# Kernel optimization log

Hardware: AMD Instinct MI355X
Metric: run time of the kernel (lower is better)

The kernel has to match this reference:

```python
import jax, jax.numpy as jnp
import numpy as np

T, B = 128, 512
OBS_DIM = 512
HIDDEN = 512
ACTION_DIM = 18
LN_EPS = 1e-6  # flax LayerNorm default


def _layer_norm(x, scale, bias):
    m = jnp.mean(x, axis=-1, keepdims=True)
    v = jnp.var(x, axis=-1, keepdims=True)
    return (x - m) * jax.lax.rsqrt(v + LN_EPS) * scale + bias


def setup_inputs() -> dict:
    key = jax.random.key(0)
    ks = jax.random.split(key, 16)
    sc = lambda k, sh: jax.random.normal(k, sh, jnp.float32) * (1.0 / np.sqrt(sh[0]))
    d = {}
    d['hidden'] = jax.random.normal(ks[0], (B, HIDDEN), jnp.float32)
    d['obs'] = jax.random.normal(ks[1], (T, B, OBS_DIM), jnp.float32)
    d['dones'] = jax.random.randint(ks[2], (T, B), 0, 2).astype(bool)
    d['last_acts'] = jax.random.randint(ks[3], (T, B), 0, ACTION_DIM, dtype=jnp.int32)
    in0 = OBS_DIM + ACTION_DIM
    d['w0'] = sc(ks[4], (in0, HIDDEN)); d['b0'] = jnp.zeros((HIDDEN,), jnp.float32)
    d['ln0_s'] = jnp.ones((HIDDEN,), jnp.float32); d['ln0_b'] = jnp.zeros((HIDDEN,), jnp.float32)
    d['w1'] = sc(ks[5], (HIDDEN, HIDDEN)); d['b1'] = jnp.zeros((HIDDEN,), jnp.float32)
    d['ln1_s'] = jnp.ones((HIDDEN,), jnp.float32); d['ln1_b'] = jnp.zeros((HIDDEN,), jnp.float32)
    d['w_ir'] = sc(ks[6], (HIDDEN, HIDDEN)); d['b_ir'] = jnp.zeros((HIDDEN,), jnp.float32)
    d['w_iz'] = sc(ks[7], (HIDDEN, HIDDEN)); d['b_iz'] = jnp.zeros((HIDDEN,), jnp.float32)
    d['w_in'] = sc(ks[8], (HIDDEN, HIDDEN)); d['b_in'] = jnp.zeros((HIDDEN,), jnp.float32)
    d['w_hr'] = sc(ks[9], (HIDDEN, HIDDEN))
    d['w_hz'] = sc(ks[10], (HIDDEN, HIDDEN))
    d['w_hn'] = sc(ks[11], (HIDDEN, HIDDEN)); d['b_hn'] = jnp.zeros((HIDDEN,), jnp.float32)
    d['w_out'] = sc(ks[12], (HIDDEN, ACTION_DIM)); d['b_out'] = jnp.zeros((ACTION_DIM,), jnp.float32)
    return d


def reference(hidden, obs, dones, last_acts,
              w0, b0, ln0_s, ln0_b, w1, b1, ln1_s, ln1_b,
              w_ir, b_ir, w_iz, b_iz, w_in, b_in,
              w_hr, w_hz, w_hn, b_hn, w_out, b_out):
    # embed last actions and concat with obs: [T, B, obs_dim + action_dim]
    one_hot = jax.nn.one_hot(last_acts, ACTION_DIM, dtype=obs.dtype)
    x = jnp.concatenate([obs, one_hot], axis=-1)
    # MLP encoder: Dense -> LayerNorm -> relu, applied over all (T, B) at once
    x = jax.nn.relu(_layer_norm(x @ w0 + b0, ln0_s, ln0_b))
    x = jax.nn.relu(_layer_norm(x @ w1 + b1, ln1_s, ln1_b))

    # ScannedRNN: GRUCell with reset-to-zero carry on done, scanned over time
    def step(h, xs):
        xt, dt = xs  # xt: [B, H], dt: [B] bool
        h = jnp.where(dt[:, None], jnp.zeros_like(h), h)
        r = jax.nn.sigmoid(xt @ w_ir + b_ir + h @ w_hr)
        z = jax.nn.sigmoid(xt @ w_iz + b_iz + h @ w_hz)
        n = jnp.tanh(xt @ w_in + b_in + r * (h @ w_hn + b_hn))
        h_new = (1.0 - z) * n + z * h
        return h_new, h_new

    new_hidden, y = jax.lax.scan(step, hidden, (x, dones))
    q_vals = y @ w_out + b_out  # [T, B, action_dim]
    return new_hidden, q_vals
```

## Files before the change

kernel.cpp:

```cpp
#include <hip/hip_runtime.h>
#include <cstdint>
#include <cstddef>


#define TT 128
#define BBATCH 512
#define HH 512
#define MM 65536
#define AD 18
#define GSTEPS 8
#define FSTRIDE 32
#define READY_U32 1064960

typedef __attribute__((ext_vector_type(8))) short short8;
typedef __attribute__((ext_vector_type(4))) float float4v;
typedef __attribute__((ext_vector_type(4))) unsigned int uint4v;

__device__ __forceinline__ unsigned short f2bf(float f) {
  union { float f; unsigned int u; } v; v.f = f;
  unsigned int r = v.u + 0x7fffu + ((v.u >> 16) & 1u);
  return (unsigned short)(r >> 16);
}
__device__ __forceinline__ float bf2f(unsigned short h) {
  union { unsigned int u; float f; } v; v.u = ((unsigned int)h) << 16;
  return v.f;
}

__device__ __forceinline__ unsigned int load_u32_coh(const unsigned int* p) {
  unsigned int v;
  asm volatile("global_load_dword %0, %1, off sc0 sc1\n\ts_waitcnt vmcnt(0)"
               : "=v"(v) : "v"(p) : "memory");
  return v;
}
__device__ __forceinline__ void store_u32_coh(unsigned int* p, unsigned int v) {
  asm volatile("global_store_dword %0, %1, off sc0 sc1"
               :: "v"(p), "v"(v) : "memory");
}
__device__ __forceinline__ void store_u64_coh(void* p, unsigned long long v) {
  asm volatile("global_store_dwordx2 %0, %1, off sc0 sc1"
               :: "v"(p), "v"(v) : "memory");
}

typedef __attribute__((address_space(3))) unsigned int* lds_u32p;
typedef const __attribute__((address_space(1))) unsigned int* glb_u32p;
__device__ __forceinline__ void async16(void* lds, const void* g) {
  __builtin_amdgcn_global_load_lds(
      (glb_u32p)(unsigned long long)g,
      (lds_u32p)(unsigned int)(unsigned long long)lds, 16, 0, 0);
}


__global__ __launch_bounds__(256) void k_conv_obs(
    const float* __restrict__ src, unsigned short* __restrict__ dst,
    unsigned int* __restrict__ flag) {
  if (blockIdx.x == 0 && threadIdx.x == 0) *flag = 0u;
  int i = blockIdx.x * 256 + threadIdx.x;
  float4v v = ((const float4v*)src)[i];
  unsigned long long pk = (unsigned long long)f2bf(v[0])
      | ((unsigned long long)f2bf(v[1]) << 16)
      | ((unsigned long long)f2bf(v[2]) << 32)
      | ((unsigned long long)f2bf(v[3]) << 48);
  ((unsigned long long*)dst)[i] = pk;
}

__global__ __launch_bounds__(256) void k_prep_t(
    const float* __restrict__ w0, const float* __restrict__ w1,
    const float* __restrict__ wir, const float* __restrict__ wiz,
    const float* __restrict__ win,
    unsigned short* __restrict__ W0at, unsigned short* __restrict__ W1t,
    unsigned short* __restrict__ Wit) {
  int o = blockIdx.x * 256 + threadIdx.x;
  int n = o >> 9, k = o & 511;
  int z = blockIdx.y;
  const float* s = (z == 0) ? w0 : (z == 1) ? w1 : (z == 2) ? wir
                 : (z == 3) ? wiz : win;
  unsigned short b = f2bf(s[k * 512 + n]);
  if (z == 0) W0at[o] = b;
  else if (z == 1) W1t[o] = b;
  else Wit[(size_t)(z - 2) * 262144 + o] = b;
}

__global__ __launch_bounds__(256) void k_prep_whf(
    const float* __restrict__ whr, const float* __restrict__ whz,
    const float* __restrict__ whn, unsigned short* __restrict__ Whf) {
  int i = blockIdx.x * 256 + threadIdx.x;
  int k = i / 1536, n = i - k * 1536;
  const float* s = (n < 512) ? whr : (n < 1024) ? whz : whn;
  float v = s[k * 512 + (n & 511)];
  Whf[((size_t)(k >> 3) * 1536 + n) * 8 + (k & 7)] = f2bf(v);
}

__global__ __launch_bounds__(256) void k_prep_misc(
    const float* __restrict__ w0, const float* __restrict__ bir,
    const float* __restrict__ biz, const float* __restrict__ bin,
    const float* __restrict__ wout, const float* __restrict__ hidden,
    const int* __restrict__ dI,
    unsigned short* __restrict__ w0act, float* __restrict__ gib,
    unsigned short* __restrict__ WoutT, unsigned short* __restrict__ hbuf,
    unsigned int* __restrict__ flag) {
  int i = blockIdx.x * 256 + threadIdx.x;
  if (i < 9216) {
    int a = i >> 9, n = i & 511;
    w0act[i] = f2bf(w0[(512 + a) * 512 + n]);
  }
  if (i < 1536)
    gib[i] = (i < 512) ? bir[i] : (i < 1024) ? biz[i - 512] : bin[i - 1024];
  if (i < 32768) {
    int n = i >> 9, k = i & 511;
    WoutT[i] = f2bf(n < AD ? wout[k * AD + n] : 0.f);
  }
  if (i < 262144) hbuf[i] = f2bf(hidden[i]);
  if (i < 16384) { if (dI[i] & 0xFFFFFFFE) atomicOr(flag, 1u); }
}

__global__ __launch_bounds__(256) void k_zero(unsigned int* __restrict__ p) {
  int i = (blockIdx.x * 256 + threadIdx.x) * 4;
  if (i < READY_U32) *(uint4v*)(p + i) = (uint4v){0u, 0u, 0u, 0u};
}


template <int MODE>
__global__ __launch_bounds__(256) void k_gemm_bt(
    const unsigned short* __restrict__ Ab,
    const unsigned short* __restrict__ Btb,
    unsigned short* __restrict__ Cb,
    int Ndim, const float* __restrict__ bias,
    const unsigned short* __restrict__ gW,
    const int* __restrict__ acts) {
  __shared__ unsigned short As[8192];
  __shared__ unsigned short Bs[8192];
  const int tid = threadIdx.x, wave = tid >> 6, lane = tid & 63;
  const int quad = lane >> 4, l15 = lane & 15;
  const int m0 = blockIdx.x * 128, n0 = blockIdx.y * 128;
  const int mblk = (wave & 1) * 64, nblk = (wave >> 1) * 64;

  float4v acc[4][4];
#pragma unroll
  for (int a = 0; a < 4; ++a)
#pragma unroll
    for (int b = 0; b < 4; ++b) acc[a][b] = (float4v){0.f, 0.f, 0.f, 0.f};

  for (int k0 = 0; k0 < 512; k0 += 64) {
#pragma unroll
    for (int r = 0; r < 4; ++r) {
      int u = r * 256 + wave * 64 + lane;
      int ch = u >> 7, mm = u & 127;
      async16(&As[(size_t)(r * 256 + wave * 64) * 8],
              Ab + (size_t)(m0 + mm) * 512 + k0 + ch * 8);
      async16(&Bs[(size_t)(r * 256 + wave * 64) * 8],
              Btb + (size_t)(n0 + mm) * 512 + k0 + ch * 8);
    }
    __syncthreads();
#pragma unroll
    for (int kk = 0; kk < 2; ++kk) {
      short8 afr[4], bfr[4];
#pragma unroll
      for (int mi = 0; mi < 4; ++mi)
        afr[mi] = *(const short8*)
            &As[((kk * 4 + quad) * 128 + mblk + mi * 16 + l15) * 8];
#pragma unroll
      for (int ni = 0; ni < 4; ++ni)
        bfr[ni] = *(const short8*)
            &Bs[((kk * 4 + quad) * 128 + nblk + ni * 16 + l15) * 8];
#pragma unroll
      for (int mi = 0; mi < 4; ++mi)
#pragma unroll
        for (int ni = 0; ni < 4; ++ni)
          acc[mi][ni] = __builtin_amdgcn_mfma_f32_16x16x32_bf16(
              afr[mi], bfr[ni], acc[mi][ni], 0, 0, 0);
    }
    __syncthreads();
  }

#pragma unroll
  for (int mi = 0; mi < 4; ++mi) {
#pragma unroll
    for (int i = 0; i < 4; ++i) {
      int row = m0 + mblk + mi * 16 + quad * 4 + i;
      int arow = (MODE == 1) ? acts[row] : 0;
#pragma unroll
      for (int ni = 0; ni < 4; ++ni) {
        int col = n0 + nblk + ni * 16 + l15;
        float v = acc[mi][ni][i] + bias[col];
        if (MODE == 1) v += bf2f(gW[arow * 512 + col]);
        if (MODE == 2) {
          int t = row >> 9, b = row & 511;
          int c = col & 511;
          size_t dst = ((size_t)((b >> 6) * 32 + (c >> 4)) * 128 + t) * 3072
                     + (size_t)(col >> 9) * 1024 + (b & 63) * 16 + (c & 15);
          Cb[dst] = f2bf(v);
        } else {
          Cb[(size_t)row * Ndim + col] = f2bf(v);
        }
      }
    }
  }
}


__global__ __launch_bounds__(256) void k_ln_relu(
    const unsigned short* __restrict__ X, unsigned short* __restrict__ Y,
    const float* __restrict__ sc, const float* __restrict__ bi) {
  int row = blockIdx.x * 4 + (threadIdx.x >> 6);
  int lane = threadIdx.x & 63;
  uint4v u = *(const uint4v*)(X + (size_t)row * 512 + lane * 8);
  float v[8];
#pragma unroll
  for (int j = 0; j < 4; ++j) {
    v[2 * j] = bf2f((unsigned short)(u[j] & 0xffffu));
    v[2 * j + 1] = bf2f((unsigned short)(u[j] >> 16));
  }
  float s = 0.f, q = 0.f;
#pragma unroll
  for (int j = 0; j < 8; ++j) { s += v[j]; q += v[j] * v[j]; }
#pragma unroll
  for (int d = 1; d < 64; d <<= 1) {
    s += __shfl_xor(s, d, 64);
    q += __shfl_xor(q, d, 64);
  }
  float mean = s * (1.f / 512.f);
  float var = fmaxf(q * (1.f / 512.f) - mean * mean, 0.f);
  float rstd = rsqrtf(var + 1e-6f);
  float4v s0 = *(const float4v*)(sc + lane * 8);
  float4v s1 = *(const float4v*)(sc + lane * 8 + 4);
  float4v c0 = *(const float4v*)(bi + lane * 8);
  float4v c1 = *(const float4v*)(bi + lane * 8 + 4);
  uint4v w;
#pragma unroll
  for (int j = 0; j < 4; ++j) {
    float a0 = fmaxf((v[2 * j] - mean) * rstd * (j < 2 ? s0[2 * j] : s1[2 * j - 4])
                         + (j < 2 ? c0[2 * j] : c1[2 * j - 4]), 0.f);
    float a1 = fmaxf((v[2 * j + 1] - mean) * rstd
                         * (j < 2 ? s0[2 * j + 1] : s1[2 * j - 3])
                         + (j < 2 ? c0[2 * j + 1] : c1[2 * j - 3]), 0.f);
    w[j] = (unsigned int)f2bf(a0) | ((unsigned int)f2bf(a1) << 16);
  }
  *(uint4v*)(Y + (size_t)row * 512 + lane * 8) = w;
}


__global__ __launch_bounds__(256, 1) void k_gru(
    const unsigned short* __restrict__ Whf, const unsigned short* __restrict__ gin,
    const float* __restrict__ bhn, const int* __restrict__ dI,
    const unsigned char* __restrict__ dB, const unsigned int* __restrict__ flag,
    const unsigned short* __restrict__ hbuf, unsigned short* __restrict__ ybuf,
    float* __restrict__ outh, unsigned int* __restrict__ ready) {
  __shared__ __align__(16) unsigned short gin_lds[2][GSTEPS * 3 * 64 * 16];
  __shared__ unsigned char d_lds[TT * 64];

  const int tid = threadIdx.x, wave = tid >> 6, lane = tid & 63;
  const int quad = lane >> 4, l15 = lane & 15;
  const int rt = blockIdx.x & 7;
  const int cc = blockIdx.x >> 3;
  const int r0b = rt * 64;
  const int rowb = wave * 16 + l15;
  const int row = r0b + rowb;
  const int c0 = cc * 16 + quad * 4;
  const int bytemode = (int)(*flag);
  const float4v bhn4 = *(const float4v*)(bhn + c0);

  const unsigned short* gsrc = gin + (size_t)(rt * 32 + cc) * 128 * 3072;

  auto stage_gin = [&](int buf, int t0) {
    const unsigned short* src = gsrc + (size_t)t0 * 3072;
#pragma unroll
    for (int r = 0; r < 12; ++r) {
      async16(&gin_lds[buf][(size_t)(r * 256 + wave * 64) * 8],
              src + (size_t)(r * 256 + tid) * 8);
    }
  };

  stage_gin(0, 0);
#pragma unroll
  for (int r = 0; r < 32; ++r) {
    int idx = r * 256 + tid;
    int t = idx >> 6, rr = idx & 63;
    int gidx = t * 512 + r0b + rr;
    d_lds[idx] = bytemode ? dB[gidx] : (unsigned char)(dI[gidx] != 0);
  }

  short8 bw[3][16];
#pragma unroll
  for (int kc = 0; kc < 16; ++kc)
#pragma unroll
    for (int g = 0; g < 3; ++g) {
      size_t u = (size_t)(kc * 4 + quad) * 1536 + (g * 512 + cc * 16 + l15);
      bw[g][kc] = *(const short8*)(Whf + u * 8);
    }

  float hprev[4];
  {
    unsigned long long w = *(const unsigned long long*)(hbuf + (size_t)row * 512 + c0);
#pragma unroll
    for (int i = 0; i < 4; ++i) hprev[i] = bf2f((unsigned short)(w >> (16 * i)));
  }

  __syncthreads();

  for (int t = 0; t < TT; ++t) {
    if (t > 0) {
      if (wave == 0) {
        const unsigned int* fp =
            ready + (((size_t)rt * 130 + t) * 32 + (lane & 31)) * FSTRIDE;
        unsigned int v;
        int guard = 0;
        do {
          v = load_u32_coh(fp);
        } while (__ballot(v == 0u) != 0ull && ++guard < (1 << 22));
      }
      __syncthreads();
      asm volatile("" ::: "memory");
    }

    const unsigned short* hsrc =
        (t == 0) ? hbuf : ybuf + (size_t)(t - 1) * 262144;
    const unsigned short* ap = hsrc + (size_t)row * 512 + quad * 8;
    short8 af[16];
#pragma unroll
    for (int kc = 0; kc < 16; ++kc) af[kc] = *(const short8*)(ap + kc * 32);

    const int dd = (int)d_lds[(t << 6) + rowb];
    if (dd) {
      const short8 z8 = {0, 0, 0, 0, 0, 0, 0, 0};
#pragma unroll
      for (int kc = 0; kc < 16; ++kc) af[kc] = z8;
    }

    if ((t & (GSTEPS - 1)) == 0 && t + GSTEPS < TT)
      stage_gin(((t >> 3) + 1) & 1, t + GSTEPS);

    const int sl = t & (GSTEPS - 1), bufc = (t >> 3) & 1;
    float gr[4], gz[4], gn[4];
    {
      const unsigned short* gl =
          &gin_lds[bufc][((size_t)(sl * 3) * 64 + rowb) * 16 + quad * 4];
      unsigned long long w0 = *(const unsigned long long*)(gl);
      unsigned long long w1 = *(const unsigned long long*)(gl + 1024);
      unsigned long long w2 = *(const unsigned long long*)(gl + 2048);
#pragma unroll
      for (int i = 0; i < 4; ++i) {
        gr[i] = bf2f((unsigned short)(w0 >> (16 * i)));
        gz[i] = bf2f((unsigned short)(w1 >> (16 * i)));
        gn[i] = bf2f((unsigned short)(w2 >> (16 * i)));
      }
    }

    float4v a0 = {0.f, 0.f, 0.f, 0.f}, a1 = a0, a2 = a0;
#pragma unroll
    for (int kc = 0; kc < 16; ++kc) {
      a0 = __builtin_amdgcn_mfma_f32_16x16x32_bf16(bw[0][kc], af[kc], a0, 0, 0, 0);
      a1 = __builtin_amdgcn_mfma_f32_16x16x32_bf16(bw[1][kc], af[kc], a1, 0, 0, 0);
      a2 = __builtin_amdgcn_mfma_f32_16x16x32_bf16(bw[2][kc], af[kc], a2, 0, 0, 0);
    }

    unsigned short* ydst = ybuf + (size_t)t * 262144;
    float hv[4];
#pragma unroll
    for (int i = 0; i < 4; ++i) {
      float hold = dd ? 0.f : hprev[i];
      float r = 1.f / (1.f + __expf(-(a0[i] + gr[i])));
      float z = 1.f / (1.f + __expf(-(a1[i] + gz[i])));
      float npre = gn[i] + r * (a2[i] + bhn4[i]);
      float n = 1.f - 2.f / (1.f + __expf(2.f * npre));
      hv[i] = (1.f - z) * n + z * hold;
      hprev[i] = hv[i];
    }
    {
      unsigned long long pk = (unsigned long long)f2bf(hv[0])
          | ((unsigned long long)f2bf(hv[1]) << 16)
          | ((unsigned long long)f2bf(hv[2]) << 32)
          | ((unsigned long long)f2bf(hv[3]) << 48);
      store_u64_coh(ydst + (size_t)row * 512 + c0, pk);
    }
    if (t == TT - 1) {
      float4v o = {hv[0], hv[1], hv[2], hv[3]};
      *(float4v*)(outh + (size_t)row * 512 + c0) = o;
    }

    __syncthreads();
    if (tid == 0)
      store_u32_coh(&ready[(((size_t)rt * 130 + t + 1) * 32 + cc) * FSTRIDE], 1u);
  }
}


__global__ __launch_bounds__(256) void k_qout(
    const unsigned short* __restrict__ Yb, const unsigned short* __restrict__ Wt,
    const float* __restrict__ bout, float* __restrict__ Q) {
  __shared__ unsigned short As[8192];
  __shared__ unsigned short Bs[4096];
  const int tid = threadIdx.x, wave = tid >> 6, lane = tid & 63;
  const int quad = lane >> 4, l15 = lane & 15;
  const int m0 = blockIdx.x * 128;

  float4v acc[2][4];
#pragma unroll
  for (int a = 0; a < 2; ++a)
#pragma unroll
    for (int b = 0; b < 4; ++b) acc[a][b] = (float4v){0.f, 0.f, 0.f, 0.f};

  for (int k0 = 0; k0 < 512; k0 += 64) {
#pragma unroll
    for (int r = 0; r < 4; ++r) {
      int u = r * 256 + wave * 64 + lane;
      int ch = u >> 7, mm = u & 127;
      async16(&As[(size_t)(r * 256 + wave * 64) * 8],
              Yb + (size_t)(m0 + mm) * 512 + k0 + ch * 8);
    }
#pragma unroll
    for (int r = 0; r < 2; ++r) {
      int u = r * 256 + wave * 64 + lane;
      int ch = u >> 6, nn = u & 63;
      async16(&Bs[(size_t)(r * 256 + wave * 64) * 8],
              Wt + (size_t)nn * 512 + k0 + ch * 8);
    }
    __syncthreads();
#pragma unroll
    for (int kk = 0; kk < 2; ++kk) {
      short8 afr[2], bfr[4];
#pragma unroll
      for (int mi = 0; mi < 2; ++mi)
        afr[mi] = *(const short8*)
            &As[((kk * 4 + quad) * 128 + wave * 32 + mi * 16 + l15) * 8];
#pragma unroll
      for (int ni = 0; ni < 4; ++ni)
        bfr[ni] = *(const short8*)
            &Bs[((kk * 4 + quad) * 64 + ni * 16 + l15) * 8];
#pragma unroll
      for (int mi = 0; mi < 2; ++mi)
#pragma unroll
        for (int ni = 0; ni < 4; ++ni)
          acc[mi][ni] = __builtin_amdgcn_mfma_f32_16x16x32_bf16(
              afr[mi], bfr[ni], acc[mi][ni], 0, 0, 0);
    }
    __syncthreads();
  }
#pragma unroll
  for (int mi = 0; mi < 2; ++mi)
#pragma unroll
    for (int ni = 0; ni < 4; ++ni)
#pragma unroll
      for (int i = 0; i < 4; ++i) {
        int row = m0 + wave * 32 + mi * 16 + quad * 4 + i;
        int colq = ni * 16 + l15;
        if (colq < AD) Q[(size_t)row * AD + colq] = acc[mi][ni][i] + bout[colq];
      }
}


extern "C" void kernel_launch(void* const* d_in, const int* in_sizes, int n_in,
                              void* d_out, int out_size, void* d_ws,
                              size_t ws_size, hipStream_t stream) {
  const float* hidden = (const float*)d_in[0];
  const float* obs = (const float*)d_in[1];
  const void* dones = d_in[2];
  const int* acts = (const int*)d_in[3];
  const float* w0 = (const float*)d_in[4];
  const float* b0 = (const float*)d_in[5];
  const float* ln0s = (const float*)d_in[6];
  const float* ln0b = (const float*)d_in[7];
  const float* w1 = (const float*)d_in[8];
  const float* b1 = (const float*)d_in[9];
  const float* ln1s = (const float*)d_in[10];
  const float* ln1b = (const float*)d_in[11];
  const float* wir = (const float*)d_in[12];
  const float* bir = (const float*)d_in[13];
  const float* wiz = (const float*)d_in[14];
  const float* biz = (const float*)d_in[15];
  const float* win = (const float*)d_in[16];
  const float* bin = (const float*)d_in[17];
  const float* whr = (const float*)d_in[18];
  const float* whz = (const float*)d_in[19];
  const float* whn = (const float*)d_in[20];
  const float* bhn = (const float*)d_in[21];
  const float* wout = (const float*)d_in[22];
  const float* bout = (const float*)d_in[23];

  char* ws = (char*)d_ws;
  unsigned short* bufA = (unsigned short*)(ws);
  unsigned short* bufB = (unsigned short*)(ws + 67108864ULL);
  unsigned short* gin = (unsigned short*)(ws + 134217728ULL);
  char* D = ws + 134217728ULL + 201326592ULL;
  unsigned short* W0at = (unsigned short*)(D);
  unsigned short* W1t = (unsigned short*)(D + 524288);
  unsigned short* Wit = (unsigned short*)(D + 1048576);
  unsigned short* Whf = (unsigned short*)(D + 2621440);
  unsigned short* WoutT = (unsigned short*)(D + 4194304);
  unsigned short* w0act = (unsigned short*)(D + 4259840);
  float* gib = (float*)(D + 4292608);
  unsigned short* hbuf = (unsigned short*)(D + 4300800);
  unsigned int* flag = (unsigned int*)(D + 4825088);
  unsigned int* ready = (unsigned int*)ws;

  (void)in_sizes; (void)n_in; (void)out_size; (void)ws_size;

  k_conv_obs<<<32768, 256, 0, stream>>>(obs, bufA, flag);
  k_prep_t<<<dim3(1024, 5), 256, 0, stream>>>(w0, w1, wir, wiz, win, W0at, W1t, Wit);
  k_prep_whf<<<3072, 256, 0, stream>>>(whr, whz, whn, Whf);
  k_prep_misc<<<1024, 256, 0, stream>>>(w0, bir, biz, bin, wout, hidden,
                                        (const int*)dones, w0act, gib, WoutT,
                                        hbuf, flag);
  k_gemm_bt<1><<<dim3(512, 4), 256, 0, stream>>>(bufA, W0at, bufB, 512, b0, w0act, acts);
  k_ln_relu<<<16384, 256, 0, stream>>>(bufB, bufA, ln0s, ln0b);
  k_gemm_bt<0><<<dim3(512, 4), 256, 0, stream>>>(bufA, W1t, bufB, 512, b1, nullptr, nullptr);
  k_ln_relu<<<16384, 256, 0, stream>>>(bufB, bufA, ln1s, ln1b);
  k_gemm_bt<2><<<dim3(512, 12), 256, 0, stream>>>(bufA, Wit, gin, 1536, gib, nullptr, nullptr);
  k_zero<<<1041, 256, 0, stream>>>(ready);
  k_gru<<<256, 256, 0, stream>>>(Whf, gin, bhn, (const int*)dones,
                                 (const unsigned char*)dones, flag, hbuf, bufB,
                                 (float*)d_out, ready);
  k_qout<<<512, 256, 0, stream>>>(bufB, WoutT, bout, (float*)d_out + 262144);
}
```

Measured before the change: 1.255 ms.

## Fuse LayerNorm+ReLU into encoder GEMMs with full-row 128x512 tiles

Replaces the 128x128-tile GEMM plus separate LayerNorm kernels with a 512-thread kernel where each block computes a full 128x512 output row-tile. This lets the LayerNorm statistics be reduced in-block through shared memory and the ReLU applied before writing, so the bf16 intermediate no longer makes an extra round trip through global memory and two launches disappear. The trade-off is a larger B tile in LDS (about 64KB plus 16KB for A), more accumulator registers per thread, one block per CU and fewer blocks in flight.

```diff
diff --git a/kernel.cpp b/kernel.cpp
--- a/kernel.cpp
+++ b/kernel.cpp
@@ -120,122 +120,156 @@
 
 
 template <int MODE>
-__global__ __launch_bounds__(256) void k_gemm_bt(
+__global__ __launch_bounds__(512, 1) void k_enc(
     const unsigned short* __restrict__ Ab,
     const unsigned short* __restrict__ Btb,
     unsigned short* __restrict__ Cb,
-    int Ndim, const float* __restrict__ bias,
+    const float* __restrict__ bias,
+    const float* __restrict__ lnS, const float* __restrict__ lnB,
     const unsigned short* __restrict__ gW,
     const int* __restrict__ acts) {
   __shared__ unsigned short As[8192];
-  __shared__ unsigned short Bs[8192];
+  __shared__ unsigned short Bs[32768];
+  __shared__ float part[128][4][2];
+  __shared__ float stats[128][2];
+
   const int tid = threadIdx.x, wave = tid >> 6, lane = tid & 63;
   const int quad = lane >> 4, l15 = lane & 15;
-  const int m0 = blockIdx.x * 128, n0 = blockIdx.y * 128;
-  const int mblk = (wave & 1) * 64, nblk = (wave >> 1) * 64;
-
-  float4v acc[4][4];
+  const int wm = wave >> 2, wn = wave & 3;
+  const int m0 = blockIdx.x * 128;
+  const int g = (MODE == 2) ? blockIdx.y : 0;
+  const unsigned short* Bt = Btb + (size_t)g * 262144;
+  const float* bi = bias + g * 512;
+
+  float4v acc[4][8];
 #pragma unroll
   for (int a = 0; a < 4; ++a)
 #pragma unroll
-    for (int b = 0; b < 4; ++b) acc[a][b] = (float4v){0.f, 0.f, 0.f, 0.f};
+    for (int b = 0; b < 8; ++b) acc[a][b] = (float4v){0.f, 0.f, 0.f, 0.f};
 
   for (int k0 = 0; k0 < 512; k0 += 64) {
 #pragma unroll
-    for (int r = 0; r < 4; ++r) {
-      int u = r * 256 + wave * 64 + lane;
+    for (int r = 0; r < 2; ++r) {
+      int u = r * 512 + tid;
       int ch = u >> 7, mm = u & 127;
-      async16(&As[(size_t)(r * 256 + wave * 64) * 8],
+      async16(&As[(size_t)(r * 512 + wave * 64) * 8],
               Ab + (size_t)(m0 + mm) * 512 + k0 + ch * 8);
-      async16(&Bs[(size_t)(r * 256 + wave * 64) * 8],
-              Btb + (size_t)(n0 + mm) * 512 + k0 + ch * 8);
+    }
+#pragma unroll
+    for (int r = 0; r < 8; ++r) {
+      int u = r * 512 + tid;
+      int ch = u >> 9, nn = u & 511;
+      async16(&Bs[(size_t)(r * 512 + wave * 64) * 8],
+              Bt + (size_t)nn * 512 + k0 + ch * 8);
     }
     __syncthreads();
 #pragma unroll
     for (int kk = 0; kk < 2; ++kk) {
-      short8 afr[4], bfr[4];
+      short8 afr[4], bfr[8];
 #pragma unroll
       for (int mi = 0; mi < 4; ++mi)
         afr[mi] = *(const short8*)
-            &As[((kk * 4 + quad) * 128 + mblk + mi * 16 + l15) * 8];
-#pragma unroll
-      for (int ni = 0; ni < 4; ++ni)
+            &As[((kk * 4 + quad) * 128 + wm * 64 + mi * 16 + l15) * 8];
+#pragma unroll
+      for (int ni = 0; ni < 8; ++ni)
         bfr[ni] = *(const short8*)
-            &Bs[((kk * 4 + quad) * 128 + nblk + ni * 16 + l15) * 8];
+            &Bs[((kk * 4 + quad) * 512 + wn * 128 + ni * 16 + l15) * 8];
 #pragma unroll
       for (int mi = 0; mi < 4; ++mi)
 #pragma unroll
-        for (int ni = 0; ni < 4; ++ni)
+        for (int ni = 0; ni < 8; ++ni)
           acc[mi][ni] = __builtin_amdgcn_mfma_f32_16x16x32_bf16(
               afr[mi], bfr[ni], acc[mi][ni], 0, 0, 0);
     }
     __syncthreads();
   }
 
-#pragma unroll
-  for (int mi = 0; mi < 4; ++mi) {
+  float bcol[8];
+#pragma unroll
+  for (int ni = 0; ni < 8; ++ni) bcol[ni] = bi[wn * 128 + ni * 16 + l15];
+#pragma unroll
+  for (int mi = 0; mi < 4; ++mi)
 #pragma unroll
     for (int i = 0; i < 4; ++i) {
-      int row = m0 + mblk + mi * 16 + quad * 4 + i;
-      int arow = (MODE == 1) ? acts[row] : 0;
-#pragma unroll
-      for (int ni = 0; ni < 4; ++ni) {
-        int col = n0 + nblk + ni * 16 + l15;
-        float v = acc[mi][ni][i] + bias[col];
-        if (MODE == 1) v += bf2f(gW[arow * 512 + col]);
-        if (MODE == 2) {
-          int t = row >> 9, b = row & 511;
-          int c = col & 511;
+      int row = m0 + wm * 64 + mi * 16 + quad * 4 + i;
+      int arow = (MODE == 0) ? acts[row] : 0;
+#pragma unroll
+      for (int ni = 0; ni < 8; ++ni) {
+        float v = acc[mi][ni][i] + bcol[ni];
+        if (MODE == 0) v += bf2f(gW[arow * 512 + wn * 128 + ni * 16 + l15]);
+        acc[mi][ni][i] = v;
+      }
+    }
+
+  if (MODE <= 1) {
+#pragma unroll
+    for (int mi = 0; mi < 4; ++mi)
+#pragma unroll
+      for (int i = 0; i < 4; ++i) {
+        float s = 0.f, q = 0.f;
+#pragma unroll
+        for (int ni = 0; ni < 8; ++ni) {
+          float v = acc[mi][ni][i];
+          s += v; q += v * v;
+        }
+#pragma unroll
+        for (int d = 1; d < 16; d <<= 1) {
+          s += __shfl_xor(s, d, 64);
+          q += __shfl_xor(q, d, 64);
+        }
+        if (l15 == 0) {
+          int rowl = wm * 64 + mi * 16 + quad * 4 + i;
+          part[rowl][wn][0] = s;
+          part[rowl][wn][1] = q;
+        }
+      }
+    __syncthreads();
+    if (tid < 128) {
+      float s = part[tid][0][0] + part[tid][1][0] + part[tid][2][0] + part[tid][3][0];
+      float q = part[tid][0][1] + part[tid][1][1] + part[tid][2][1] + part[tid][3][1];
+      float mean = s * (1.f / 512.f);
+      float var = fmaxf(q * (1.f / 512.f) - mean * mean, 0.f);
+      stats[tid][0] = mean;
+      stats[tid][1] = rsqrtf(var + 1e-6f);
+    }
+    __syncthreads();
+    float sc8[8], cb8[8];
+#pragma unroll
+    for (int ni = 0; ni < 8; ++ni) {
+      int col = wn * 128 + ni * 16 + l15;
+      sc8[ni] = lnS[col];
+      cb8[ni] = lnB[col];
+    }
+#pragma unroll
+    for (int mi = 0; mi < 4; ++mi)
+#pragma unroll
+      for (int i = 0; i < 4; ++i) {
+        int rowl = wm * 64 + mi * 16 + quad * 4 + i;
+        float mean = stats[rowl][0], rstd = stats[rowl][1];
+        int row = m0 + rowl;
+#pragma unroll
+        for (int ni = 0; ni < 8; ++ni) {
+          int col = wn * 128 + ni * 16 + l15;
+          float v = fmaxf((acc[mi][ni][i] - mean) * rstd * sc8[ni] + cb8[ni], 0.f);
+          Cb[(size_t)row * 512 + col] = f2bf(v);
+        }
+      }
+  } else {
+#pragma unroll
+    for (int mi = 0; mi < 4; ++mi)
+#pragma unroll
+      for (int i = 0; i < 4; ++i) {
+        int row = m0 + wm * 64 + mi * 16 + quad * 4 + i;
+        int t = row >> 9, b = row & 511;
+#pragma unroll
+        for (int ni = 0; ni < 8; ++ni) {
+          int c = wn * 128 + ni * 16 + l15;
           size_t dst = ((size_t)((b >> 6) * 32 + (c >> 4)) * 128 + t) * 3072
-                     + (size_t)(col >> 9) * 1024 + (b & 63) * 16 + (c & 15);
-          Cb[dst] = f2bf(v);
-        } else {
-          Cb[(size_t)row * Ndim + col] = f2bf(v);
+                     + (size_t)g * 1024 + (b & 63) * 16 + (c & 15);
+          Cb[dst] = f2bf(acc[mi][ni][i]);
         }
       }
-    }
-  }
-}
-
-
-__global__ __launch_bounds__(256) void k_ln_relu(
-    const unsigned short* __restrict__ X, unsigned short* __restrict__ Y,
-    const float* __restrict__ sc, const float* __restrict__ bi) {
-  int row = blockIdx.x * 4 + (threadIdx.x >> 6);
-  int lane = threadIdx.x & 63;
-  uint4v u = *(const uint4v*)(X + (size_t)row * 512 + lane * 8);
-  float v[8];
-#pragma unroll
-  for (int j = 0; j < 4; ++j) {
-    v[2 * j] = bf2f((unsigned short)(u[j] & 0xffffu));
-    v[2 * j + 1] = bf2f((unsigned short)(u[j] >> 16));
-  }
-  float s = 0.f, q = 0.f;
-#pragma unroll
-  for (int j = 0; j < 8; ++j) { s += v[j]; q += v[j] * v[j]; }
-#pragma unroll
-  for (int d = 1; d < 64; d <<= 1) {
-    s += __shfl_xor(s, d, 64);
-    q += __shfl_xor(q, d, 64);
-  }
-  float mean = s * (1.f / 512.f);
-  float var = fmaxf(q * (1.f / 512.f) - mean * mean, 0.f);
-  float rstd = rsqrtf(var + 1e-6f);
-  float4v s0 = *(const float4v*)(sc + lane * 8);
-  float4v s1 = *(const float4v*)(sc + lane * 8 + 4);
-  float4v c0 = *(const float4v*)(bi + lane * 8);
-  float4v c1 = *(const float4v*)(bi + lane * 8 + 4);
-  uint4v w;
-#pragma unroll
-  for (int j = 0; j < 4; ++j) {
-    float a0 = fmaxf((v[2 * j] - mean) * rstd * (j < 2 ? s0[2 * j] : s1[2 * j - 4])
-                         + (j < 2 ? c0[2 * j] : c1[2 * j - 4]), 0.f);
-    float a1 = fmaxf((v[2 * j + 1] - mean) * rstd
-                         * (j < 2 ? s0[2 * j + 1] : s1[2 * j - 3])
-                         + (j < 2 ? c0[2 * j + 1] : c1[2 * j - 3]), 0.f);
-    w[j] = (unsigned int)f2bf(a0) | ((unsigned int)f2bf(a1) << 16);
-  }
-  *(uint4v*)(Y + (size_t)row * 512 + lane * 8) = w;
+  }
 }
 
 
@@ -500,11 +534,10 @@
   k_prep_misc<<<1024, 256, 0, stream>>>(w0, bir, biz, bin, wout, hidden,
                                         (const int*)dones, w0act, gib, WoutT,
                                         hbuf, flag);
-  k_gemm_bt<1><<<dim3(512, 4), 256, 0, stream>>>(bufA, W0at, bufB, 512, b0, w0act, acts);
-  k_ln_relu<<<16384, 256, 0, stream>>>(bufB, bufA, ln0s, ln0b);
-  k_gemm_bt<0><<<dim3(512, 4), 256, 0, stream>>>(bufA, W1t, bufB, 512, b1, nullptr, nullptr);
-  k_ln_relu<<<16384, 256, 0, stream>>>(bufB, bufA, ln1s, ln1b);
-  k_gemm_bt<2><<<dim3(512, 12), 256, 0, stream>>>(bufA, Wit, gin, 1536, gib, nullptr, nullptr);
+  k_enc<0><<<512, 512, 0, stream>>>(bufA, W0at, bufB, b0, ln0s, ln0b, w0act, acts);
+  k_enc<1><<<512, 512, 0, stream>>>(bufB, W1t, bufA, b1, ln1s, ln1b, nullptr, nullptr);
+  k_enc<2><<<dim3(512, 3), 512, 0, stream>>>(bufA, Wit, gin, gib, nullptr, nullptr,
+                                             nullptr, nullptr);
   k_zero<<<1041, 256, 0, stream>>>(ready);
   k_gru<<<256, 256, 0, stream>>>(Whf, gin, bhn, (const int*)dones,
                                  (const unsigned char*)dones, flag, hbuf, bufB,
```

New measurement: 1.230 ms. No clear change (-2.0%).
